# Kernel tuning notes

Measured on AMD Instinct MI355X. Metric: run time of the kernel, lower is better.

Reference implementation:

```python
import jax, jax.numpy as jnp
import numpy as np

N, D, E, R, K = 8192, 1024, 8, 16, 2  # tokens, d_model, experts, lora rank, top_k


def setup_inputs() -> dict:
    key = jax.random.key(0)
    ks = jax.random.split(key, 6)
    s = 1.0 / np.sqrt(D)
    return {
        "x": jax.random.normal(ks[0], (N, D), jnp.float32),
        "W_gate": jax.random.normal(ks[1], (E, D), jnp.float32) * s,
        "A": jax.random.normal(ks[2], (E, D, R), jnp.float32) * s,
        "B": jax.random.normal(ks[3], (E, R, D), jnp.float32) * (1.0 / np.sqrt(R)),
        "W_base": jax.random.normal(ks[4], (D, D), jnp.float32) * s,
        "b_base": jax.random.normal(ks[5], (D,), jnp.float32) * 0.01,
    }


def reference(x, W_gate, A, B, W_base, b_base):
    # Gating: logits [N, E] -> top-k values/indices, softmax over the k slots
    logits = x @ W_gate.T
    topk_vals, topk_idx = jax.lax.top_k(logits, K)          # [N, K]
    w = jax.nn.softmax(topk_vals.astype(jnp.float32), axis=1).astype(x.dtype)
    # Dense combine weights [N, E]: weight for expert e if selected, else 0
    combine = jnp.sum(jax.nn.one_hot(topk_idx, E, dtype=x.dtype) * w[..., None], axis=1)
    # LoRA experts: expert_e(x) = x @ A_e @ B_e; weighted scatter-add fused via einsum
    h = jnp.einsum('nd,edr->enr', x, A)                     # [E, N, R]
    moe_out = jnp.einsum('enr,erd,ne->nd', h, B, combine)   # [N, D]
    # Base (shared) linear expert, always added when lora_experts=True
    base = x @ W_base.T + b_base
    return moe_out + base
```

## Files before the change

kernel.cpp:

```cpp
#include <hip/hip_runtime.h>
#include <stdint.h>

#define NTOK 8192
#define DM   1024
#define NE   8
#define NR   16
#define KX   1152

typedef short bf16x8 __attribute__((ext_vector_type(8)));
typedef float f32x4  __attribute__((ext_vector_type(4)));

__device__ __forceinline__ unsigned short f2bf(float f) {
    union { float f; unsigned u; } v; v.f = f;
    unsigned r = v.u + 0x7fffu + ((v.u >> 16) & 1u);
    return (unsigned short)(r >> 16);
}

__device__ __forceinline__ void gld16(const void* g, void* l) {
    __builtin_amdgcn_global_load_lds((__attribute__((address_space(1))) void*)g,
                                     (__attribute__((address_space(3))) void*)l,
                                     16, 0, 0);
}

__global__ __launch_bounds__(256) void prep(const float* __restrict__ x,
                                            const float* __restrict__ Wg,
                                            const float* __restrict__ Asrc,
                                            const float* __restrict__ Bsrc,
                                            const float* __restrict__ Wb,
                                            float* __restrict__ combine,
                                            unsigned short* __restrict__ Xext,
                                            unsigned short* __restrict__ WBext,
                                            unsigned short* __restrict__ At) {
    const int b = blockIdx.x;
    const int t = threadIdx.x;

    if (b < 2048) {
        const int lane = t & 63;
        const int w = t >> 6;
        const int n = b * 4 + w;

        const float4* x4 = (const float4*)(x + (size_t)n * DM);
        float4 xv[4];
        #pragma unroll
        for (int i = 0; i < 4; ++i) xv[i] = x4[i * 64 + lane];

        float acc[NE];
        #pragma unroll
        for (int e = 0; e < NE; ++e) {
            const float4* wg4 = (const float4*)(Wg + (size_t)e * DM);
            float s = 0.f;
            #pragma unroll
            for (int i = 0; i < 4; ++i) {
                float4 g = wg4[i * 64 + lane];
                s += xv[i].x * g.x + xv[i].y * g.y + xv[i].z * g.z + xv[i].w * g.w;
            }
            acc[e] = s;
        }
        #pragma unroll
        for (int off = 32; off >= 1; off >>= 1) {
            #pragma unroll
            for (int e = 0; e < NE; ++e) acc[e] += __shfl_xor(acc[e], off, 64);
        }
        float best = acc[0]; int bi = 0;
        #pragma unroll
        for (int e = 1; e < NE; ++e) if (acc[e] > best) { best = acc[e]; bi = e; }
        float sec = -1e30f; int si = 0;
        #pragma unroll
        for (int e = 0; e < NE; ++e) if (e != bi && acc[e] > sec) { sec = acc[e]; si = e; }
        const float ed = __expf(sec - best);
        const float w0 = 1.f / (1.f + ed);
        const float w1 = ed * w0;
        if (lane < NE)
            combine[n * NE + lane] = (lane == bi) ? w0 : ((lane == si) ? w1 : 0.f);

        unsigned short* xrow = Xext + (size_t)n * KX;
        #pragma unroll
        for (int i = 0; i < 4; ++i) {
            ushort4 o;
            o.x = f2bf(xv[i].x); o.y = f2bf(xv[i].y);
            o.z = f2bf(xv[i].z); o.w = f2bf(xv[i].w);
            *(ushort4*)(xrow + (i * 64 + lane) * 4) = o;
        }
    } else if (b < 3072) {
        const int j = b - 2048;
        unsigned short* row = WBext + (size_t)j * KX;
        float4 v = ((const float4*)(Wb + (size_t)j * DM))[t];
        ushort4 o;
        o.x = f2bf(v.x); o.y = f2bf(v.y); o.z = f2bf(v.z); o.w = f2bf(v.w);
        *(ushort4*)(row + t * 4) = o;
        if (t < 128) row[DM + t] = f2bf(Bsrc[(size_t)t * DM + j]);
    } else {
        const int p = b - 3072;
        const int e = p >> 4, r = p & 15;
        for (int d = t; d < DM; d += 256)
            At[(size_t)p * DM + d] = f2bf(Asrc[e * (DM * NR) + d * NR + r]);
    }
}

__global__ __launch_bounds__(256) void hall_kernel(unsigned short* Xext,
                                                   const unsigned short* __restrict__ At,
                                                   const float* __restrict__ combine) {
    __shared__ __align__(16) unsigned short lds[(32 + 128) * 64];
    const int t = threadIdx.x;
    const int lane = t & 63;
    const int w = t >> 6;
    const int quad = lane >> 4;
    const int l15 = lane & 15;
    const int bm = blockIdx.x;

    const int srow = t >> 3;
    const int seg  = (t & 7) ^ (srow & 7);

    f32x4 acc[2][2] = {};
    const unsigned short* gA = Xext + (size_t)(bm * 32 + srow) * KX + seg * 8;

    for (int k0 = 0; k0 < DM; k0 += 64) {
        __syncthreads();
        gld16(gA + k0, (char*)lds + w * 1024);
        #pragma unroll
        for (int r = 0; r < 4; ++r) {
            const unsigned short* g = At + (size_t)(r * 32 + srow) * DM + k0 + seg * 8;
            gld16(g, (char*)lds + 4096 + r * 4096 + w * 1024);
        }
        __syncthreads();
        #pragma unroll
        for (int kk = 0; kk < 2; ++kk) {
            const int gs = kk * 4 + quad;
            const int sw = (gs ^ (l15 & 7)) * 8;
            bf16x8 a[2], bb[2];
            #pragma unroll
            for (int i = 0; i < 2; ++i)
                a[i] = *(const bf16x8*)&lds[(i * 16 + l15) * 64 + sw];
            #pragma unroll
            for (int jf = 0; jf < 2; ++jf)
                bb[jf] = *(const bf16x8*)&lds[2048 + (w * 32 + jf * 16 + l15) * 64 + sw];
            #pragma unroll
            for (int i = 0; i < 2; ++i)
                #pragma unroll
                for (int jf = 0; jf < 2; ++jf)
                    acc[i][jf] = __builtin_amdgcn_mfma_f32_16x16x32_bf16(a[i], bb[jf], acc[i][jf], 0, 0, 0);
        }
    }
    #pragma unroll
    for (int i = 0; i < 2; ++i)
        #pragma unroll
        for (int jf = 0; jf < 2; ++jf) {
            const int p = w * 32 + jf * 16 + l15;
            const int e = p >> 4;
            #pragma unroll
            for (int v = 0; v < 4; ++v) {
                const int n = bm * 32 + i * 16 + quad * 4 + v;
                const float val = acc[i][jf][v] * combine[n * NE + e];
                Xext[(size_t)n * KX + DM + p] = f2bf(val);
            }
        }
}

__global__ __launch_bounds__(256, 2) void mgemm(const unsigned short* __restrict__ Xext,
                                                const unsigned short* __restrict__ WBext,
                                                const float* __restrict__ bias,
                                                float* __restrict__ out) {
    __shared__ __align__(16) unsigned short lds[32768];
    const int t = threadIdx.x;
    const int lane = t & 63;
    const int w = t >> 6;
    const int quad = lane >> 4;
    const int l15 = lane & 15;

    const int bid = blockIdx.x;
    const int xcd = bid & 7;
    const int loc = bid >> 3;
    const int bm = xcd * 8 + (loc & 7);
    const int bn = loc >> 3;

    const int wm = (w & 1) * 64;
    const int wn = (w >> 1) * 64;

    f32x4 acc[4][4] = {};

    const int srow = w * 4 + (lane >> 4);
    const int seg  = (lane & 15) ^ (srow & 7);
    const unsigned short* gA = Xext  + (size_t)(bm * 128 + srow) * KX + seg * 8;
    const unsigned short* gB = WBext + (size_t)(bn * 128 + srow) * KX + seg * 8;
    char* ldsA = (char*)lds + w * 1024;
    char* ldsB = (char*)lds + 32768 + w * 1024;

    for (int k0 = 0; k0 < KX; k0 += 128) {
        __syncthreads();
        #pragma unroll
        for (int c = 0; c < 8; ++c) {
            gld16(gA + (size_t)c * 16 * KX + k0, ldsA + c * 4096);
            gld16(gB + (size_t)c * 16 * KX + k0, ldsB + c * 4096);
        }
        __syncthreads();
        #pragma unroll
        for (int kk = 0; kk < 4; ++kk) {
            const int gs = kk * 4 + quad;
            const int sw = (gs ^ (l15 & 7)) * 8;
            bf16x8 a[4], b[4];
            #pragma unroll
            for (int i = 0; i < 4; ++i)
                a[i] = *(const bf16x8*)&lds[(wm + i * 16 + l15) * 128 + sw];
            #pragma unroll
            for (int j = 0; j < 4; ++j)
                b[j] = *(const bf16x8*)&lds[16384 + (wn + j * 16 + l15) * 128 + sw];
            #pragma unroll
            for (int i = 0; i < 4; ++i)
                #pragma unroll
                for (int j = 0; j < 4; ++j)
                    acc[i][j] = __builtin_amdgcn_mfma_f32_16x16x32_bf16(a[i], b[j], acc[i][j], 0, 0, 0);
        }
    }

    __syncthreads();
    float* lf = (float*)lds + w * 4096;
    #pragma unroll
    for (int j = 0; j < 4; ++j) {
        const float bv = bias[bn * 128 + wn + j * 16 + l15];
        #pragma unroll
        for (int i = 0; i < 4; ++i)
            #pragma unroll
            for (int v = 0; v < 4; ++v) {
                const int row_l = i * 16 + quad * 4 + v;
                const int col_s = (j * 16 + l15) ^ ((row_l & 1) << 4);
                lf[row_l * 64 + col_s] = acc[i][j][v] + bv;
            }
    }
    __builtin_amdgcn_s_waitcnt(0);
    #pragma unroll
    for (int r = 0; r < 16; ++r) {
        const int row_r = r * 4 + (lane >> 4);
        const int col4  = (lane & 15) * 4;
        const int col4s = col4 ^ ((row_r & 1) << 4);
        float4 vv = *(const float4*)&lf[row_r * 64 + col4s];
        *(float4*)&out[(size_t)(bm * 128 + wm + row_r) * DM + bn * 128 + wn + col4] = vv;
    }
}

extern "C" void kernel_launch(void* const* d_in, const int* in_sizes, int n_in,
                              void* d_out, int out_size, void* d_ws, size_t ws_size,
                              hipStream_t stream) {
    const float* x  = (const float*)d_in[0];
    const float* Wg = (const float*)d_in[1];
    const float* A  = (const float*)d_in[2];
    const float* B  = (const float*)d_in[3];
    const float* Wb = (const float*)d_in[4];
    const float* bb = (const float*)d_in[5];
    float* out = (float*)d_out;

    char* ws = (char*)d_ws;
    float*          combine = (float*)ws;
    unsigned short* Xext    = (unsigned short*)(ws + 262144);
    unsigned short* WBext   = (unsigned short*)(ws + 262144 + 18874368);
    unsigned short* At      = (unsigned short*)(ws + 262144 + 18874368 + 2359296);

    hipLaunchKernelGGL(prep,        dim3(3200), dim3(256), 0, stream,
                       x, Wg, A, B, Wb, combine, Xext, WBext, At);
    hipLaunchKernelGGL(hall_kernel, dim3(256),  dim3(256), 0, stream, Xext, At, combine);
    hipLaunchKernelGGL(mgemm,       dim3(512),  dim3(256), 0, stream, Xext, WBext, bb, out);
}
```

Baseline: 134.9 us.

## Fuse gating and x bf16 conversion into the LoRA hidden kernel

Result: slower. 143.2 us (+6.2%).

```diff
diff --git a/kernel.cpp b/kernel.cpp
--- a/kernel.cpp
+++ b/kernel.cpp
@@ -22,67 +22,15 @@
                                      16, 0, 0);
 }
 
-__global__ __launch_bounds__(256) void prep(const float* __restrict__ x,
-                                            const float* __restrict__ Wg,
-                                            const float* __restrict__ Asrc,
-                                            const float* __restrict__ Bsrc,
-                                            const float* __restrict__ Wb,
-                                            float* __restrict__ combine,
-                                            unsigned short* __restrict__ Xext,
-                                            unsigned short* __restrict__ WBext,
-                                            unsigned short* __restrict__ At) {
+__global__ __launch_bounds__(256) void wprep(const float* __restrict__ Asrc,
+                                             const float* __restrict__ Bsrc,
+                                             const float* __restrict__ Wb,
+                                             unsigned short* __restrict__ WBext,
+                                             unsigned short* __restrict__ At) {
     const int b = blockIdx.x;
     const int t = threadIdx.x;
-
-    if (b < 2048) {
-        const int lane = t & 63;
-        const int w = t >> 6;
-        const int n = b * 4 + w;
-
-        const float4* x4 = (const float4*)(x + (size_t)n * DM);
-        float4 xv[4];
-        #pragma unroll
-        for (int i = 0; i < 4; ++i) xv[i] = x4[i * 64 + lane];
-
-        float acc[NE];
-        #pragma unroll
-        for (int e = 0; e < NE; ++e) {
-            const float4* wg4 = (const float4*)(Wg + (size_t)e * DM);
-            float s = 0.f;
-            #pragma unroll
-            for (int i = 0; i < 4; ++i) {
-                float4 g = wg4[i * 64 + lane];
-                s += xv[i].x * g.x + xv[i].y * g.y + xv[i].z * g.z + xv[i].w * g.w;
-            }
-            acc[e] = s;
-        }
-        #pragma unroll
-        for (int off = 32; off >= 1; off >>= 1) {
-            #pragma unroll
-            for (int e = 0; e < NE; ++e) acc[e] += __shfl_xor(acc[e], off, 64);
-        }
-        float best = acc[0]; int bi = 0;
-        #pragma unroll
-        for (int e = 1; e < NE; ++e) if (acc[e] > best) { best = acc[e]; bi = e; }
-        float sec = -1e30f; int si = 0;
-        #pragma unroll
-        for (int e = 0; e < NE; ++e) if (e != bi && acc[e] > sec) { sec = acc[e]; si = e; }
-        const float ed = __expf(sec - best);
-        const float w0 = 1.f / (1.f + ed);
-        const float w1 = ed * w0;
-        if (lane < NE)
-            combine[n * NE + lane] = (lane == bi) ? w0 : ((lane == si) ? w1 : 0.f);
-
-        unsigned short* xrow = Xext + (size_t)n * KX;
-        #pragma unroll
-        for (int i = 0; i < 4; ++i) {
-            ushort4 o;
-            o.x = f2bf(xv[i].x); o.y = f2bf(xv[i].y);
-            o.z = f2bf(xv[i].z); o.w = f2bf(xv[i].w);
-            *(ushort4*)(xrow + (i * 64 + lane) * 4) = o;
-        }
-    } else if (b < 3072) {
-        const int j = b - 2048;
+    if (b < 1024) {
+        const int j = b;
         unsigned short* row = WBext + (size_t)j * KX;
         float4 v = ((const float4*)(Wb + (size_t)j * DM))[t];
         ushort4 o;
@@ -90,37 +38,66 @@
         *(ushort4*)(row + t * 4) = o;
         if (t < 128) row[DM + t] = f2bf(Bsrc[(size_t)t * DM + j]);
     } else {
-        const int p = b - 3072;
+        const int p = b - 1024;
         const int e = p >> 4, r = p & 15;
         for (int d = t; d < DM; d += 256)
             At[(size_t)p * DM + d] = f2bf(Asrc[e * (DM * NR) + d * NR + r]);
     }
 }
 
-__global__ __launch_bounds__(256) void hall_kernel(unsigned short* Xext,
-                                                   const unsigned short* __restrict__ At,
-                                                   const float* __restrict__ combine) {
-    __shared__ __align__(16) unsigned short lds[(32 + 128) * 64];
+__global__ __launch_bounds__(256) void gmoe(const float* __restrict__ x,
+                                            const float* __restrict__ Wg,
+                                            const unsigned short* __restrict__ At,
+                                            unsigned short* __restrict__ Xext) {
+    __shared__ __align__(16) unsigned short lds[2048 + 8192 + 512];
+    unsigned short* xt = lds;
+    unsigned short* at = lds + 2048;
+    float* comb = (float*)(lds + 2048 + 8192);
+
     const int t = threadIdx.x;
     const int lane = t & 63;
     const int w = t >> 6;
     const int quad = lane >> 4;
     const int l15 = lane & 15;
     const int bm = blockIdx.x;
-
-    const int srow = t >> 3;
-    const int seg  = (t & 7) ^ (srow & 7);
+    const int n0 = bm * 32;
+
+    const int r   = t >> 3;
+    const int c8  = t & 7;
+    const int seg = c8 ^ (r & 7);
+
+    const int srow2 = t >> 3;
+    const int gseg  = (t & 7) ^ (srow2 & 7);
 
     f32x4 acc[2][2] = {};
-    const unsigned short* gA = Xext + (size_t)(bm * 32 + srow) * KX + seg * 8;
+    float gl[NE] = {};
+
+    const float* xp = x + (size_t)(n0 + r) * DM + seg * 8;
 
     for (int k0 = 0; k0 < DM; k0 += 64) {
         __syncthreads();
-        gld16(gA + k0, (char*)lds + w * 1024);
-        #pragma unroll
-        for (int r = 0; r < 4; ++r) {
-            const unsigned short* g = At + (size_t)(r * 32 + srow) * DM + k0 + seg * 8;
-            gld16(g, (char*)lds + 4096 + r * 4096 + w * 1024);
+        float4 u0 = *(const float4*)(xp + k0);
+        float4 u1 = *(const float4*)(xp + k0 + 4);
+        #pragma unroll
+        for (int e = 0; e < NE; ++e) {
+            const float* wp = Wg + (size_t)e * DM + k0 + seg * 8;
+            float4 g0 = *(const float4*)wp;
+            float4 g1 = *(const float4*)(wp + 4);
+            gl[e] += u0.x * g0.x + u0.y * g0.y + u0.z * g0.z + u0.w * g0.w
+                   + u1.x * g1.x + u1.y * g1.y + u1.z * g1.z + u1.w * g1.w;
+        }
+        ushort4 b0, b1;
+        b0.x = f2bf(u0.x); b0.y = f2bf(u0.y); b0.z = f2bf(u0.z); b0.w = f2bf(u0.w);
+        b1.x = f2bf(u1.x); b1.y = f2bf(u1.y); b1.z = f2bf(u1.z); b1.w = f2bf(u1.w);
+        *(ushort4*)&xt[r * 64 + c8 * 8]     = b0;
+        *(ushort4*)&xt[r * 64 + c8 * 8 + 4] = b1;
+        unsigned short* gx = Xext + (size_t)(n0 + r) * KX + k0 + seg * 8;
+        *(ushort4*)gx       = b0;
+        *(ushort4*)(gx + 4) = b1;
+        #pragma unroll
+        for (int rr = 0; rr < 4; ++rr) {
+            const unsigned short* g = At + (size_t)(rr * 32 + srow2) * DM + k0 + gseg * 8;
+            gld16(g, (char*)at + rr * 4096 + w * 1024);
         }
         __syncthreads();
         #pragma unroll
@@ -130,10 +107,10 @@
             bf16x8 a[2], bb[2];
             #pragma unroll
             for (int i = 0; i < 2; ++i)
-                a[i] = *(const bf16x8*)&lds[(i * 16 + l15) * 64 + sw];
+                a[i] = *(const bf16x8*)&xt[(i * 16 + l15) * 64 + sw];
             #pragma unroll
             for (int jf = 0; jf < 2; ++jf)
-                bb[jf] = *(const bf16x8*)&lds[2048 + (w * 32 + jf * 16 + l15) * 64 + sw];
+                bb[jf] = *(const bf16x8*)&at[(w * 32 + jf * 16 + l15) * 64 + sw];
             #pragma unroll
             for (int i = 0; i < 2; ++i)
                 #pragma unroll
@@ -141,17 +118,36 @@
                     acc[i][jf] = __builtin_amdgcn_mfma_f32_16x16x32_bf16(a[i], bb[jf], acc[i][jf], 0, 0, 0);
         }
     }
+
+    #pragma unroll
+    for (int off = 1; off <= 4; off <<= 1)
+        #pragma unroll
+        for (int e = 0; e < NE; ++e) gl[e] += __shfl_xor(gl[e], off, 64);
+    {
+        float best = gl[0]; int bi = 0;
+        #pragma unroll
+        for (int e = 1; e < NE; ++e) if (gl[e] > best) { best = gl[e]; bi = e; }
+        float sec = -1e30f; int si = 0;
+        #pragma unroll
+        for (int e = 0; e < NE; ++e) if (e != bi && gl[e] > sec) { sec = gl[e]; si = e; }
+        const float ed = __expf(sec - best);
+        const float w0 = 1.f / (1.f + ed);
+        const float w1 = ed * w0;
+        comb[r * NE + c8] = (c8 == bi) ? w0 : ((c8 == si) ? w1 : 0.f);
+    }
+    __syncthreads();
+
     #pragma unroll
     for (int i = 0; i < 2; ++i)
         #pragma unroll
         for (int jf = 0; jf < 2; ++jf) {
-            const int p = w * 32 + jf * 16 + l15;
-            const int e = p >> 4;
+            const int col = w * 32 + jf * 16 + l15;
+            const int e = col >> 4;
             #pragma unroll
             for (int v = 0; v < 4; ++v) {
-                const int n = bm * 32 + i * 16 + quad * 4 + v;
-                const float val = acc[i][jf][v] * combine[n * NE + e];
-                Xext[(size_t)n * KX + DM + p] = f2bf(val);
+                const int nl = i * 16 + quad * 4 + v;
+                const float val = acc[i][jf][v] * comb[nl * NE + e];
+                Xext[(size_t)(n0 + nl) * KX + DM + col] = f2bf(val);
             }
         }
 }
@@ -228,8 +224,8 @@
     }
     __builtin_amdgcn_s_waitcnt(0);
     #pragma unroll
-    for (int r = 0; r < 16; ++r) {
-        const int row_r = r * 4 + (lane >> 4);
+    for (int rr = 0; rr < 16; ++rr) {
+        const int row_r = rr * 4 + (lane >> 4);
         const int col4  = (lane & 15) * 4;
         const int col4s = col4 ^ ((row_r & 1) << 4);
         float4 vv = *(const float4*)&lf[row_r * 64 + col4s];
@@ -249,13 +245,11 @@
     float* out = (float*)d_out;
 
     char* ws = (char*)d_ws;
-    float*          combine = (float*)ws;
-    unsigned short* Xext    = (unsigned short*)(ws + 262144);
-    unsigned short* WBext   = (unsigned short*)(ws + 262144 + 18874368);
-    unsigned short* At      = (unsigned short*)(ws + 262144 + 18874368 + 2359296);
-
-    hipLaunchKernelGGL(prep,        dim3(3200), dim3(256), 0, stream,
-                       x, Wg, A, B, Wb, combine, Xext, WBext, At);
-    hipLaunchKernelGGL(hall_kernel, dim3(256),  dim3(256), 0, stream, Xext, At, combine);
-    hipLaunchKernelGGL(mgemm,       dim3(512),  dim3(256), 0, stream, Xext, WBext, bb, out);
-}
+    unsigned short* Xext  = (unsigned short*)ws;
+    unsigned short* WBext = (unsigned short*)(ws + 18874368);
+    unsigned short* At    = (unsigned short*)(ws + 18874368 + 2359296);
+
+    hipLaunchKernelGGL(wprep, dim3(1152), dim3(256), 0, stream, A, B, Wb, WBext, At);
+    hipLaunchKernelGGL(gmoe,  dim3(256),  dim3(256), 0, stream, x, Wg, At, Xext);
+    hipLaunchKernelGGL(mgemm, dim3(512),  dim3(256), 0, stream, Xext, WBext, bb, out);
+}
```

## Double-buffer LDS tiles in both GEMMs and split hall kernel across column halves

Applied to the files above, without the earlier changes.

After: 129.1 us. -4.2%, faster.

```diff
diff --git a/kernel.cpp b/kernel.cpp
--- a/kernel.cpp
+++ b/kernel.cpp
@@ -100,60 +100,72 @@
 __global__ __launch_bounds__(256) void hall_kernel(unsigned short* Xext,
                                                    const unsigned short* __restrict__ At,
                                                    const float* __restrict__ combine) {
-    __shared__ __align__(16) unsigned short lds[(32 + 128) * 64];
+    __shared__ __align__(16) unsigned short lds[12288];
     const int t = threadIdx.x;
     const int lane = t & 63;
     const int w = t >> 6;
     const int quad = lane >> 4;
     const int l15 = lane & 15;
-    const int bm = blockIdx.x;
+    const int bid = blockIdx.x;
+    const int bm = bid >> 1;
+    const int cb = bid & 1;
+    const int n0 = bm * 32;
+    const int wm = (w & 1) * 16;
+    const int wn = (w >> 1) * 32;
 
     const int srow = t >> 3;
     const int seg  = (t & 7) ^ (srow & 7);
 
-    f32x4 acc[2][2] = {};
-    const unsigned short* gA = Xext + (size_t)(bm * 32 + srow) * KX + seg * 8;
-
-    for (int k0 = 0; k0 < DM; k0 += 64) {
-        __syncthreads();
-        gld16(gA + k0, (char*)lds + w * 1024);
-        #pragma unroll
-        for (int r = 0; r < 4; ++r) {
-            const unsigned short* g = At + (size_t)(r * 32 + srow) * DM + k0 + seg * 8;
-            gld16(g, (char*)lds + 4096 + r * 4096 + w * 1024);
-        }
-        __syncthreads();
-        #pragma unroll
-        for (int kk = 0; kk < 2; ++kk) {
-            const int gs = kk * 4 + quad;
-            const int sw = (gs ^ (l15 & 7)) * 8;
-            bf16x8 a[2], bb[2];
-            #pragma unroll
-            for (int i = 0; i < 2; ++i)
-                a[i] = *(const bf16x8*)&lds[(i * 16 + l15) * 64 + sw];
-            #pragma unroll
-            for (int jf = 0; jf < 2; ++jf)
-                bb[jf] = *(const bf16x8*)&lds[2048 + (w * 32 + jf * 16 + l15) * 64 + sw];
-            #pragma unroll
-            for (int i = 0; i < 2; ++i)
-                #pragma unroll
-                for (int jf = 0; jf < 2; ++jf)
-                    acc[i][jf] = __builtin_amdgcn_mfma_f32_16x16x32_bf16(a[i], bb[jf], acc[i][jf], 0, 0, 0);
-        }
-    }
+    const unsigned short* gX  = Xext + (size_t)(n0 + srow) * KX + seg * 8;
+    const unsigned short* gA0 = At + (size_t)(cb * 64 + srow) * DM + seg * 8;
+    const unsigned short* gA1 = At + (size_t)(cb * 64 + 32 + srow) * DM + seg * 8;
+
+    f32x4 acc[2] = {};
+
+    #define HALL_STAGE(k0, s)                                              \
+        gld16(gX  + (k0), (char*)lds + (s) * 12288 + w * 1024);            \
+        gld16(gA0 + (k0), (char*)lds + (s) * 12288 + 4096 + w * 1024);     \
+        gld16(gA1 + (k0), (char*)lds + (s) * 12288 + 8192 + w * 1024);
+
+    #define HALL_COMPUTE(s)                                                        \
+        {                                                                          \
+            const int xo = (s) * 6144, ao = (s) * 6144 + 2048;                     \
+            _Pragma("unroll")                                                      \
+            for (int kk = 0; kk < 2; ++kk) {                                       \
+                const int gs = kk * 4 + quad;                                      \
+                const int sw = (gs ^ (l15 & 7)) * 8;                               \
+                bf16x8 a = *(const bf16x8*)&lds[xo + (wm + l15) * 64 + sw];        \
+                _Pragma("unroll")                                                  \
+                for (int jf = 0; jf < 2; ++jf) {                                   \
+                    bf16x8 bb = *(const bf16x8*)&lds[ao + (wn + jf * 16 + l15) * 64 + sw]; \
+                    acc[jf] = __builtin_amdgcn_mfma_f32_16x16x32_bf16(a, bb, acc[jf], 0, 0, 0); \
+                }                                                                  \
+            }                                                                      \
+        }
+
+    HALL_STAGE(0, 0);
+    for (int k0 = 0; k0 < DM; k0 += 128) {
+        __syncthreads();
+        HALL_STAGE(k0 + 64, 1);
+        HALL_COMPUTE(0);
+        __syncthreads();
+        if (k0 + 128 < DM) { HALL_STAGE(k0 + 128, 0); }
+        HALL_COMPUTE(1);
+    }
+
     #pragma unroll
-    for (int i = 0; i < 2; ++i)
-        #pragma unroll
-        for (int jf = 0; jf < 2; ++jf) {
-            const int p = w * 32 + jf * 16 + l15;
-            const int e = p >> 4;
-            #pragma unroll
-            for (int v = 0; v < 4; ++v) {
-                const int n = bm * 32 + i * 16 + quad * 4 + v;
-                const float val = acc[i][jf][v] * combine[n * NE + e];
-                Xext[(size_t)n * KX + DM + p] = f2bf(val);
-            }
-        }
+    for (int jf = 0; jf < 2; ++jf) {
+        const int p = cb * 64 + wn + jf * 16 + l15;
+        const int e = p >> 4;
+        #pragma unroll
+        for (int v = 0; v < 4; ++v) {
+            const int n = n0 + wm + quad * 4 + v;
+            const float val = acc[jf][v] * combine[n * NE + e];
+            Xext[(size_t)n * KX + DM + p] = f2bf(val);
+        }
+    }
+    #undef HALL_STAGE
+    #undef HALL_COMPUTE
 }
 
 __global__ __launch_bounds__(256, 2) void mgemm(const unsigned short* __restrict__ Xext,
@@ -178,39 +190,51 @@
 
     f32x4 acc[4][4] = {};
 
-    const int srow = w * 4 + (lane >> 4);
-    const int seg  = (lane & 15) ^ (srow & 7);
+    const int srow = t >> 3;
+    const int seg  = (t & 7) ^ (srow & 7);
     const unsigned short* gA = Xext  + (size_t)(bm * 128 + srow) * KX + seg * 8;
     const unsigned short* gB = WBext + (size_t)(bn * 128 + srow) * KX + seg * 8;
-    char* ldsA = (char*)lds + w * 1024;
-    char* ldsB = (char*)lds + 32768 + w * 1024;
-
+
+    #define MG_STAGE(k0, s)                                                          \
+        _Pragma("unroll")                                                            \
+        for (int c = 0; c < 4; ++c) {                                                \
+            gld16(gA + (size_t)c * 32 * KX + (k0), (char*)lds + (s) * 32768 + c * 4096 + w * 1024);        \
+            gld16(gB + (size_t)c * 32 * KX + (k0), (char*)lds + (s) * 32768 + 16384 + c * 4096 + w * 1024);\
+        }
+
+    #define MG_COMPUTE(s)                                                            \
+        {                                                                            \
+            const int ao = (s) * 16384, bo = (s) * 16384 + 8192;                     \
+            _Pragma("unroll")                                                        \
+            for (int kk = 0; kk < 2; ++kk) {                                         \
+                const int gs = kk * 4 + quad;                                        \
+                const int sw = (gs ^ (l15 & 7)) * 8;                                 \
+                bf16x8 a[4], b[4];                                                   \
+                _Pragma("unroll")                                                    \
+                for (int i = 0; i < 4; ++i)                                          \
+                    a[i] = *(const bf16x8*)&lds[ao + (wm + i * 16 + l15) * 64 + sw]; \
+                _Pragma("unroll")                                                    \
+                for (int j = 0; j < 4; ++j)                                          \
+                    b[j] = *(const bf16x8*)&lds[bo + (wn + j * 16 + l15) * 64 + sw]; \
+                _Pragma("unroll")                                                    \
+                for (int i = 0; i < 4; ++i)                                          \
+                    _Pragma("unroll")                                                \
+                    for (int j = 0; j < 4; ++j)                                      \
+                        acc[i][j] = __builtin_amdgcn_mfma_f32_16x16x32_bf16(a[i], b[j], acc[i][j], 0, 0, 0); \
+            }                                                                        \
+        }
+
+    MG_STAGE(0, 0);
     for (int k0 = 0; k0 < KX; k0 += 128) {
         __syncthreads();
-        #pragma unroll
-        for (int c = 0; c < 8; ++c) {
-            gld16(gA + (size_t)c * 16 * KX + k0, ldsA + c * 4096);
-            gld16(gB + (size_t)c * 16 * KX + k0, ldsB + c * 4096);
-        }
-        __syncthreads();
-        #pragma unroll
-        for (int kk = 0; kk < 4; ++kk) {
-            const int gs = kk * 4 + quad;
-            const int sw = (gs ^ (l15 & 7)) * 8;
-            bf16x8 a[4], b[4];
-            #pragma unroll
-            for (int i = 0; i < 4; ++i)
-                a[i] = *(const bf16x8*)&lds[(wm + i * 16 + l15) * 128 + sw];
-            #pragma unroll
-            for (int j = 0; j < 4; ++j)
-                b[j] = *(const bf16x8*)&lds[16384 + (wn + j * 16 + l15) * 128 + sw];
-            #pragma unroll
-            for (int i = 0; i < 4; ++i)
-                #pragma unroll
-                for (int j = 0; j < 4; ++j)
-                    acc[i][j] = __builtin_amdgcn_mfma_f32_16x16x32_bf16(a[i], b[j], acc[i][j], 0, 0, 0);
-        }
-    }
+        MG_STAGE(k0 + 64, 1);
+        MG_COMPUTE(0);
+        __syncthreads();
+        if (k0 + 128 < KX) { MG_STAGE(k0 + 128, 0); }
+        MG_COMPUTE(1);
+    }
+    #undef MG_STAGE
+    #undef MG_COMPUTE
 
     __syncthreads();
     float* lf = (float*)lds + w * 4096;
@@ -228,8 +252,8 @@
     }
     __builtin_amdgcn_s_waitcnt(0);
     #pragma unroll
-    for (int r = 0; r < 16; ++r) {
-        const int row_r = r * 4 + (lane >> 4);
+    for (int rr = 0; rr < 16; ++rr) {
+        const int row_r = rr * 4 + (lane >> 4);
         const int col4  = (lane & 15) * 4;
         const int col4s = col4 ^ ((row_r & 1) << 4);
         float4 vv = *(const float4*)&lf[row_r * 64 + col4s];
@@ -256,6 +280,6 @@
 
     hipLaunchKernelGGL(prep,        dim3(3200), dim3(256), 0, stream,
                        x, Wg, A, B, Wb, combine, Xext, WBext, At);
-    hipLaunchKernelGGL(hall_kernel, dim3(256),  dim3(256), 0, stream, Xext, At, combine);
+    hipLaunchKernelGGL(hall_kernel, dim3(512),  dim3(256), 0, stream, Xext, At, combine);
     hipLaunchKernelGGL(mgemm,       dim3(512),  dim3(256), 0, stream, Xext, WBext, bb, out);
 }
```
